# Performance work log

Measured on AMD Instinct MI355X. Metric: run time of the kernel, lower is better.

The kernel has to match this reference:

```python
import jax, jax.numpy as jnp
import numpy as np

N, NFEAT, NHID, NCLASS = 8192, 512, 256, 2
ALPHA = 0.5


def setup_inputs() -> dict:
    key = jax.random.key(0)
    k1, k2, k3, k4, k5 = jax.random.split(key, 5)
    x = jax.random.normal(k1, (N, NFEAT), dtype=jnp.float32)
    adj = jax.random.uniform(k2, (N, N), dtype=jnp.float32)
    # GraphConvolution init: uniform(-stdv, stdv), stdv = 1/sqrt(out_features)
    s1 = 1.0 / np.sqrt(NHID)
    W1 = jax.random.uniform(k3, (NFEAT, NHID), dtype=jnp.float32, minval=-s1, maxval=s1)
    s2 = 1.0 / np.sqrt(NCLASS)
    W2 = jax.random.uniform(k4, (NHID, NCLASS), dtype=jnp.float32, minval=-s2, maxval=s2)
    b2 = jax.random.uniform(k5, (NCLASS,), dtype=jnp.float32, minval=-s2, maxval=s2)
    return {"x": x, "adj": adj, "W1": W1, "W2": W2, "b2": b2}


def _mid_filter_2(adj, alpha):
    # D_row = diag(rowsum^-0.5), D_col = diag(colsum^-0.5); inf -> 0
    d_row = jnp.power(jnp.sum(adj, axis=1), -0.5)
    d_row = jnp.where(jnp.isinf(d_row), 0.0, d_row)
    d_col = jnp.power(jnp.sum(adj, axis=0), -0.5)
    d_col = jnp.where(jnp.isinf(d_col), 0.0, d_col)
    # (adj @ D_col)^T @ D_row)^T == d_row[:,None] * adj * d_col[None,:]
    DAD = d_row[:, None] * adj * d_col[None, :]
    I = jnp.eye(adj.shape[0], dtype=adj.dtype)
    return jnp.matmul(alpha * I - DAD, I + DAD)


def reference(x, adj, W1, W2, b2):
    adj_f = _mid_filter_2(adj, ALPHA)
    # hidden layer (no bias): relu(adj_f @ (x @ W1)); dropout = identity (eval)
    h = jax.nn.relu(jnp.matmul(adj_f, jnp.matmul(x, W1)))
    # output layer (with bias)
    out = jnp.matmul(adj_f, jnp.matmul(h, W2)) + b2
    return jax.nn.log_softmax(out, axis=-1)
```

## Files before the change

kernel.cpp:

```cpp
#include <hip/hip_runtime.h>
#include <hip/hip_bf16.h>

typedef unsigned short u16;
typedef unsigned int u32;
typedef __attribute__((ext_vector_type(8))) short short8;
typedef __attribute__((ext_vector_type(4))) float f32x4;

#define NN 8192
#define NF 512
#define NH 256
#define SPLITZ 8
#define RB 256

__device__ __forceinline__ float bf2f(u32 u) {
  union { u32 i; float f; } v; v.i = u << 16; return v.f;
}
__device__ __forceinline__ u16 f2bf(float f) {
  union { __hip_bfloat16 b; u16 u; } v; v.b = __float2bfloat16(f); return v.u;
}
__device__ __forceinline__ u32 pack2(float a, float b) {
  return (u32)f2bf(a) | ((u32)f2bf(b) << 16);
}

__global__ __launch_bounds__(256) void conv_adj_k(const float* __restrict__ adj,
                                                  u16* __restrict__ adjb,
                                                  float* __restrict__ rowsum_part,
                                                  float* __restrict__ colsum_part) {
  __shared__ float red[4][32];
  const int t = threadIdx.x;
  const int w = t >> 6, lane = t & 63;
  const int s = blockIdx.x;
  const int c0 = s * 2048 + t * 8;
  const int r0 = blockIdx.y * 32;
  float cp[8] = {0.f, 0.f, 0.f, 0.f, 0.f, 0.f, 0.f, 0.f};
  for (int r = 0; r < 32; ++r) {
    const size_t base = (size_t)(r0 + r) * NN + c0;
    float4 v0 = *(const float4*)(adj + base);
    float4 v1 = *(const float4*)(adj + base + 4);
    uint4 pk;
    pk.x = pack2(v0.x, v0.y); pk.y = pack2(v0.z, v0.w);
    pk.z = pack2(v1.x, v1.y); pk.w = pack2(v1.z, v1.w);
    *(uint4*)(adjb + base) = pk;
    cp[0] += v0.x; cp[1] += v0.y; cp[2] += v0.z; cp[3] += v0.w;
    cp[4] += v1.x; cp[5] += v1.y; cp[6] += v1.z; cp[7] += v1.w;
    float rs = (v0.x + v0.y) + (v0.z + v0.w) + ((v1.x + v1.y) + (v1.z + v1.w));
#pragma unroll
    for (int off = 32; off > 0; off >>= 1) rs += __shfl_down(rs, off, 64);
    if (lane == 0) red[w][r] = rs;
  }
  __syncthreads();
  if (t < 32)
    rowsum_part[(size_t)s * NN + r0 + t] =
        (red[0][t] + red[1][t]) + (red[2][t] + red[3][t]);
  float* cdst = colsum_part + (size_t)blockIdx.y * NN + c0;
  *(float4*)cdst = make_float4(cp[0], cp[1], cp[2], cp[3]);
  *(float4*)(cdst + 4) = make_float4(cp[4], cp[5], cp[6], cp[7]);
}

__global__ __launch_bounds__(256) void reduce_sums_k(const float* __restrict__ rowp,
                                                     const float* __restrict__ colp,
                                                     float* __restrict__ drow,
                                                     float* __restrict__ dcol) {
  const int i = blockIdx.x * 256 + threadIdx.x;
  const float rs = (rowp[i] + rowp[NN + i]) + (rowp[2 * NN + i] + rowp[3 * NN + i]);
  drow[i] = (rs > 0.f) ? rsqrtf(rs) : 0.f;
  float cs = 0.f;
#pragma unroll 8
  for (int rb = 0; rb < RB; ++rb) cs += colp[(size_t)rb * NN + i];
  dcol[i] = (cs > 0.f) ? rsqrtf(cs) : 0.f;
}

__global__ __launch_bounds__(256) void convx_k(const float* __restrict__ x,
                                               u16* __restrict__ xb) {
  const size_t i = ((size_t)blockIdx.x * 256 + threadIdx.x) * 8;
  float4 v0 = *(const float4*)(x + i);
  float4 v1 = *(const float4*)(x + i + 4);
  uint4 pk;
  pk.x = pack2(v0.x, v0.y); pk.y = pack2(v0.z, v0.w);
  pk.z = pack2(v1.x, v1.y); pk.w = pack2(v1.z, v1.w);
  *(uint4*)(xb + i) = pk;
}

__global__ __launch_bounds__(256) void convw1_k(const float* __restrict__ in,
                                                u16* __restrict__ out) {
  __shared__ float tile[32][33];
  const int tx = threadIdx.x & 31, ty = threadIdx.x >> 5;
  const int c0 = blockIdx.x * 32;
  const int r0 = blockIdx.y * 32;
#pragma unroll
  for (int d = 0; d < 32; d += 8)
    tile[ty + d][tx] = in[(size_t)(r0 + ty + d) * NH + c0 + tx];
  __syncthreads();
#pragma unroll
  for (int d = 0; d < 32; d += 8)
    out[(size_t)(c0 + ty + d) * NF + r0 + tx] = f2bf(tile[tx][ty + d]);
}

__device__ __forceinline__ void stage128(const u16* __restrict__ A, int lda,
                                         const u16* __restrict__ Bt, int ldb,
                                         int m0, int n0, int kk,
                                         u16* as_, u16* bs_, int tid) {
#pragma unroll
  for (int h = 0; h < 2; ++h) {
    const int slot = tid + h * 256;
    const int row = slot >> 2, kc = slot & 3;
    const u16* srcA = A + (size_t)(m0 + row) * lda + kk + kc * 8;
    __builtin_amdgcn_global_load_lds((const __attribute__((address_space(1))) void*)srcA,
                                     (__attribute__((address_space(3))) void*)(as_ + slot * 8),
                                     16, 0, 0);
    const u16* srcB = Bt + (size_t)(n0 + row) * ldb + kk + kc * 8;
    __builtin_amdgcn_global_load_lds((const __attribute__((address_space(1))) void*)srcB,
                                     (__attribute__((address_space(3))) void*)(bs_ + slot * 8),
                                     16, 0, 0);
  }
}

__global__ __launch_bounds__(256) void gemm_k(const u16* __restrict__ A, int lda,
                                              const u16* __restrict__ Bt, int ldb,
                                              int kChunk, float* __restrict__ out) {
  __shared__ __align__(16) u16 As[2][128 * 32];
  __shared__ __align__(16) u16 Bs[2][128 * 32];
  const int tid = threadIdx.x;
  const int w = tid >> 6, lane = tid & 63;
  const int lq = lane >> 4, lr = lane & 15;
  const int wr = (w >> 1) * 64, wc = (w & 1) * 64;
  const int n0 = blockIdx.x * 128;
  const int m0 = blockIdx.y * 128;
  const int kk0 = blockIdx.z * kChunk;
  const int nk = kChunk >> 5;

  f32x4 acc[4][4] = {};

  stage128(A, lda, Bt, ldb, m0, n0, kk0, As[0], Bs[0], tid);
  for (int kt = 0; kt < nk; ++kt) {
    const int cur = kt & 1;
    __syncthreads();
    if (kt + 1 < nk)
      stage128(A, lda, Bt, ldb, m0, n0, kk0 + ((kt + 1) << 5), As[cur ^ 1], Bs[cur ^ 1], tid);
    short8 a[4], b[4];
#pragma unroll
    for (int i = 0; i < 4; ++i)
      a[i] = *(const short8*)(As[cur] + (wr + i * 16 + lr) * 32 + lq * 8);
#pragma unroll
    for (int i = 0; i < 4; ++i)
      b[i] = *(const short8*)(Bs[cur] + (wc + i * 16 + lr) * 32 + lq * 8);
#pragma unroll
    for (int i = 0; i < 4; ++i)
#pragma unroll
      for (int j = 0; j < 4; ++j)
        acc[i][j] = __builtin_amdgcn_mfma_f32_16x16x32_bf16(a[i], b[j], acc[i][j], 0, 0, 0);
  }

  float* o = out + (size_t)blockIdx.z * ((size_t)NN * NH);
#pragma unroll
  for (int i = 0; i < 4; ++i)
#pragma unroll
    for (int j = 0; j < 4; ++j) {
      const int gn = n0 + wc + j * 16 + lr;
      const int gm0 = m0 + wr + i * 16 + lq * 4;
#pragma unroll
      for (int r = 0; r < 4; ++r)
        o[(size_t)(gm0 + r) * NH + gn] = acc[i][j][r];
    }
}

__device__ __forceinline__ void stage256(const u16* __restrict__ A, int lda,
                                         const u16* __restrict__ Bt, int ldb,
                                         int m0, int kk,
                                         u16* as_, u16* bs_, int tid) {
#pragma unroll
  for (int h = 0; h < 4; ++h) {
    const int slot = tid + h * 512;
    const int row = slot >> 3, kc = (slot & 7) * 8;
    const u16* srcA = A + (size_t)(m0 + row) * lda + kk + kc;
    __builtin_amdgcn_global_load_lds((const __attribute__((address_space(1))) void*)srcA,
                                     (__attribute__((address_space(3))) void*)(as_ + slot * 8),
                                     16, 0, 0);
    const u16* srcB = Bt + (size_t)row * ldb + kk + kc;
    __builtin_amdgcn_global_load_lds((const __attribute__((address_space(1))) void*)srcB,
                                     (__attribute__((address_space(3))) void*)(bs_ + slot * 8),
                                     16, 0, 0);
  }
}

__global__ __launch_bounds__(512, 2) void gemm256_k(const u16* __restrict__ A, int lda,
                                                    const u16* __restrict__ Bt, int ldb,
                                                    int kChunk, float* __restrict__ out) {
  __shared__ __align__(16) u16 As[2][256 * 64];
  __shared__ __align__(16) u16 Bs[2][256 * 64];
  const int tid = threadIdx.x;
  const int w = tid >> 6, lane = tid & 63;
  const int lq = lane >> 4, lr = lane & 15;
  const int wr = (w >> 2) * 128;
  const int wc = (w & 3) * 64;
  const int m0 = blockIdx.x * 256;
  const int kk0 = blockIdx.y * kChunk;
  const int nk = kChunk >> 6;

  f32x4 acc[8][4] = {};

  stage256(A, lda, Bt, ldb, m0, kk0, As[0], Bs[0], tid);
  for (int kt = 0; kt < nk; ++kt) {
    const int cur = kt & 1;
    __syncthreads();
    if (kt + 1 < nk)
      stage256(A, lda, Bt, ldb, m0, kk0 + ((kt + 1) << 6), As[cur ^ 1], Bs[cur ^ 1], tid);
#pragma unroll
    for (int kk2 = 0; kk2 < 2; ++kk2) {
      short8 a[8], b[4];
#pragma unroll
      for (int i = 0; i < 8; ++i)
        a[i] = *(const short8*)(As[cur] + (wr + i * 16 + lr) * 64 + kk2 * 32 + lq * 8);
#pragma unroll
      for (int j = 0; j < 4; ++j)
        b[j] = *(const short8*)(Bs[cur] + (wc + j * 16 + lr) * 64 + kk2 * 32 + lq * 8);
#pragma unroll
      for (int i = 0; i < 8; ++i)
#pragma unroll
        for (int j = 0; j < 4; ++j)
          acc[i][j] = __builtin_amdgcn_mfma_f32_16x16x32_bf16(a[i], b[j], acc[i][j], 0, 0, 0);
    }
  }

  float* o = out + (size_t)blockIdx.y * ((size_t)NN * NH);
#pragma unroll
  for (int i = 0; i < 8; ++i)
#pragma unroll
    for (int j = 0; j < 4; ++j) {
      const int gn = wc + j * 16 + lr;
      const int gm0 = m0 + wr + i * 16 + lq * 4;
#pragma unroll
      for (int r = 0; r < 4; ++r)
        o[(size_t)(gm0 + r) * NH + gn] = acc[i][j][r];
    }
}

__global__ __launch_bounds__(256) void t1_k(const float* __restrict__ P,
                                            const float* __restrict__ dcol,
                                            u16* __restrict__ B1t) {
  __shared__ float tile[32][33];
  const int tx = threadIdx.x & 31, ty = threadIdx.x >> 5;
  const int c0 = blockIdx.x * 32;
  const int r0 = blockIdx.y * 32;
#pragma unroll
  for (int d = 0; d < 32; d += 8) {
    const int rr = r0 + ty + d;
    tile[ty + d][tx] = dcol[rr] * P[(size_t)rr * NH + c0 + tx];
  }
  __syncthreads();
#pragma unroll
  for (int d = 0; d < 32; d += 8)
    B1t[(size_t)(c0 + ty + d) * NN + r0 + tx] = f2bf(tile[tx][ty + d]);
}

__global__ __launch_bounds__(256) void r2_k(const float* __restrict__ Qp,
                                            const float* __restrict__ drow,
                                            const float* __restrict__ dcol,
                                            float* __restrict__ Q1,
                                            u16* __restrict__ B2t) {
  __shared__ float tile[32][33];
  const int tx = threadIdx.x & 31, ty = threadIdx.x >> 5;
  const int c0 = blockIdx.x * 32;
  const int r0 = blockIdx.y * 32;
  const size_t sl = (size_t)NN * NH;
#pragma unroll
  for (int d = 0; d < 32; d += 8) {
    const int rr = r0 + ty + d;
    const size_t idx = (size_t)rr * NH + c0 + tx;
    float s = 0.f;
#pragma unroll
    for (int z = 0; z < SPLITZ; ++z) s += Qp[idx + (size_t)z * sl];
    const float q = drow[rr] * s;
    Q1[idx] = q;
    tile[ty + d][tx] = dcol[rr] * q;
  }
  __syncthreads();
#pragma unroll
  for (int d = 0; d < 32; d += 8)
    B2t[(size_t)(c0 + ty + d) * NN + r0 + tx] = f2bf(tile[tx][ty + d]);
}

__global__ __launch_bounds__(256) void r3_k(const float* __restrict__ Hp,
                                            const float* __restrict__ P,
                                            const float* __restrict__ Q1,
                                            const float* __restrict__ drow,
                                            u16* __restrict__ Hb) {
  const size_t i = ((size_t)blockIdx.x * 256 + threadIdx.x) * 4;
  const int row = (int)(i >> 8);
  const size_t sl = (size_t)NN * NH;
  float4 s = make_float4(0.f, 0.f, 0.f, 0.f);
#pragma unroll
  for (int z = 0; z < SPLITZ; ++z) {
    float4 v = *(const float4*)(Hp + i + (size_t)z * sl);
    s.x += v.x; s.y += v.y; s.z += v.z; s.w += v.w;
  }
  float4 p = *(const float4*)(P + i);
  float4 q = *(const float4*)(Q1 + i);
  const float dr = drow[row];
  const float h0 = fmaxf(0.5f * p.x - 0.5f * q.x - dr * s.x, 0.f);
  const float h1 = fmaxf(0.5f * p.y - 0.5f * q.y - dr * s.y, 0.f);
  const float h2 = fmaxf(0.5f * p.z - 0.5f * q.z - dr * s.z, 0.f);
  const float h3 = fmaxf(0.5f * p.w - 0.5f * q.w - dr * s.w, 0.f);
  uint2 pk;
  pk.x = pack2(h0, h1);
  pk.y = pack2(h2, h3);
  *(uint2*)(Hb + i) = pk;
}

__global__ __launch_bounds__(256) void r_k(const u16* __restrict__ H,
                                           const float* __restrict__ W2,
                                           const float* __restrict__ dcol,
                                           float* __restrict__ R, float* __restrict__ B3) {
  const int w = threadIdx.x >> 6, lane = threadIdx.x & 63;
  const int i = blockIdx.x * 4 + w;
  uint2 hv = *(const uint2*)(H + (size_t)i * NH + lane * 4);
  float4 w01 = *(const float4*)(W2 + lane * 8);
  float4 w23 = *(const float4*)(W2 + lane * 8 + 4);
  const float h0 = bf2f(hv.x & 0xffffu), h1 = bf2f(hv.x >> 16);
  const float h2 = bf2f(hv.y & 0xffffu), h3 = bf2f(hv.y >> 16);
  float a0 = h0 * w01.x + h1 * w01.z + h2 * w23.x + h3 * w23.z;
  float a1 = h0 * w01.y + h1 * w01.w + h2 * w23.y + h3 * w23.w;
#pragma unroll
  for (int off = 32; off > 0; off >>= 1) {
    a0 += __shfl_down(a0, off, 64);
    a1 += __shfl_down(a1, off, 64);
  }
  if (lane == 0) {
    R[i * 2] = a0;
    R[i * 2 + 1] = a1;
    const float dc = dcol[i];
    B3[i * 2] = dc * a0;
    B3[i * 2 + 1] = dc * a1;
  }
}

__global__ __launch_bounds__(256) void gemv_k(
    const u16* __restrict__ adjb, const float* __restrict__ B,
    const float* __restrict__ drow, const float* __restrict__ dcol,
    const float* __restrict__ Rin, const float* __restrict__ S1in,
    const float* __restrict__ b2, float* __restrict__ S1out,
    float* __restrict__ B4, float* __restrict__ outp, int mode) {
  const int i = blockIdx.x;
  const int t = threadIdx.x;
  float a0 = 0.f, a1 = 0.f;
#pragma unroll
  for (int c = 0; c < 4; ++c) {
    const int col = c * 2048 + t * 8;
    uint4 av = *(const uint4*)(adjb + (size_t)i * NN + col);
    const u32* aw = (const u32*)&av;
    float bv[16];
    *(float4*)(bv) = *(const float4*)(B + col * 2);
    *(float4*)(bv + 4) = *(const float4*)(B + col * 2 + 4);
    *(float4*)(bv + 8) = *(const float4*)(B + col * 2 + 8);
    *(float4*)(bv + 12) = *(const float4*)(B + col * 2 + 12);
#pragma unroll
    for (int j = 0; j < 8; ++j) {
      const u32 a = aw[j >> 1];
      const float aval = bf2f((j & 1) ? (a >> 16) : (a & 0xffffu));
      a0 += aval * bv[2 * j];
      a1 += aval * bv[2 * j + 1];
    }
  }
#pragma unroll
  for (int off = 32; off > 0; off >>= 1) {
    a0 += __shfl_down(a0, off, 64);
    a1 += __shfl_down(a1, off, 64);
  }
  __shared__ float red[8];
  const int w = t >> 6, lane = t & 63;
  if (lane == 0) { red[w] = a0; red[4 + w] = a1; }
  __syncthreads();
  if (t == 0) {
    float s0 = (red[0] + red[1]) + (red[2] + red[3]);
    float s1 = (red[4] + red[5]) + (red[6] + red[7]);
    const float dr = drow[i];
    s0 *= dr; s1 *= dr;
    if (mode == 0) {
      S1out[i * 2] = s0;
      S1out[i * 2 + 1] = s1;
      const float dc = dcol[i];
      B4[i * 2] = dc * s0;
      B4[i * 2 + 1] = dc * s1;
    } else {
      const float l0 = 0.5f * Rin[i * 2] - 0.5f * S1in[i * 2] - s0 + b2[0];
      const float l1 = 0.5f * Rin[i * 2 + 1] - 0.5f * S1in[i * 2 + 1] - s1 + b2[1];
      const float m = fmaxf(l0, l1);
      const float lse = m + logf(__expf(l0 - m) + __expf(l1 - m));
      outp[i * 2] = l0 - lse;
      outp[i * 2 + 1] = l1 - lse;
    }
  }
}

extern "C" void kernel_launch(void* const* d_in, const int* in_sizes, int n_in,
                              void* d_out, int out_size, void* d_ws, size_t ws_size,
                              hipStream_t stream) {
  (void)in_sizes; (void)n_in; (void)out_size; (void)ws_size;
  const float* x   = (const float*)d_in[0];
  const float* adj = (const float*)d_in[1];
  const float* W1  = (const float*)d_in[2];
  const float* W2  = (const float*)d_in[3];
  const float* b2  = (const float*)d_in[4];
  float* outp = (float*)d_out;

  char* ws = (char*)d_ws;
  size_t off = 0;
  auto alloc = [&](size_t bytes) -> char* {
    char* p = ws + off;
    off += (bytes + 255) & ~(size_t)255;
    return p;
  };
  u16* adjb  = (u16*)alloc((size_t)NN * NN * 2);
  u16* xb    = (u16*)alloc((size_t)NN * NF * 2);
  u16* W1t   = (u16*)alloc((size_t)NH * NF * 2);
  float* rowp = (float*)alloc((size_t)4 * NN * 4);
  float* colp = (float*)alloc((size_t)RB * NN * 4);
  float* drow = (float*)alloc((size_t)NN * 4);
  float* dcol = (float*)alloc((size_t)NN * 4);
  float* P   = (float*)alloc((size_t)NN * NH * 4);
  u16* B1t   = (u16*)alloc((size_t)NH * NN * 2);
  float* Qp  = (float*)alloc((size_t)SPLITZ * NN * NH * 4);
  float* Q1  = (float*)alloc((size_t)NN * NH * 4);
  u16* B2t   = (u16*)alloc((size_t)NH * NN * 2);
  u16* Hb    = (u16*)alloc((size_t)NN * NH * 2);
  float* R   = (float*)alloc((size_t)NN * 2 * 4);
  float* B3  = (float*)alloc((size_t)NN * 2 * 4);
  float* S1  = (float*)alloc((size_t)NN * 2 * 4);
  float* B4  = (float*)alloc((size_t)NN * 2 * 4);
  float* Hp  = Qp;

  conv_adj_k<<<dim3(4, RB), 256, 0, stream>>>(adj, adjb, rowp, colp);
  reduce_sums_k<<<NN / 256, 256, 0, stream>>>(rowp, colp, drow, dcol);
  convx_k<<<2048, 256, 0, stream>>>(x, xb);
  convw1_k<<<dim3(8, 16), 256, 0, stream>>>(W1, W1t);

  gemm_k<<<dim3(2, 64, 1), 256, 0, stream>>>(xb, NF, W1t, NF, NF, P);
  t1_k<<<dim3(8, 256), 256, 0, stream>>>(P, dcol, B1t);

  gemm256_k<<<dim3(32, SPLITZ), 512, 0, stream>>>(adjb, NN, B1t, NN, NN / SPLITZ, Qp);
  r2_k<<<dim3(8, 256), 256, 0, stream>>>(Qp, drow, dcol, Q1, B2t);

  gemm256_k<<<dim3(32, SPLITZ), 512, 0, stream>>>(adjb, NN, B2t, NN, NN / SPLITZ, Hp);
  r3_k<<<2048, 256, 0, stream>>>(Hp, P, Q1, drow, Hb);

  r_k<<<NN / 4, 256, 0, stream>>>(Hb, W2, dcol, R, B3);
  gemv_k<<<NN, 256, 0, stream>>>(adjb, B3, drow, dcol, nullptr, nullptr, nullptr, S1, B4, nullptr, 0);
  gemv_k<<<NN, 256, 0, stream>>>(adjb, B4, drow, dcol, R, S1, b2, nullptr, nullptr, outp, 1);
}
```

Before: 652.8 us.

## Fuse conversion kernels, merge adj pass with x@W1 GEMM, deepen GEMM pipeline

Merges the x and W1 conversions into one launch, and runs the adj bf16 conversion with row/col sums in the same grid as the x@W1 GEMM so the two independent jobs overlap. The big adj GEMM moves to a 4-stage LDS ring with BK=32, XOR-swizzled LDS layout, explicit vmcnt waits with raw barriers, and setprio around the MFMAs. The H reduction is fused with the W2 projection, so the bf16 H round trip is gone. The hand-written waitcnt counts depend on the exact number of outstanding loads, and the smaller K step adds more barriers per tile.

```diff
diff --git a/kernel.cpp b/kernel.cpp
--- a/kernel.cpp
+++ b/kernel.cpp
@@ -11,6 +11,7 @@
 #define NH 256
 #define SPLITZ 8
 #define RB 256
+#define BKR 32
 
 __device__ __forceinline__ float bf2f(u32 u) {
   union { u32 i; float f; } v; v.i = u << 16; return v.f;
@@ -20,41 +21,6 @@
 }
 __device__ __forceinline__ u32 pack2(float a, float b) {
   return (u32)f2bf(a) | ((u32)f2bf(b) << 16);
-}
-
-__global__ __launch_bounds__(256) void conv_adj_k(const float* __restrict__ adj,
-                                                  u16* __restrict__ adjb,
-                                                  float* __restrict__ rowsum_part,
-                                                  float* __restrict__ colsum_part) {
-  __shared__ float red[4][32];
-  const int t = threadIdx.x;
-  const int w = t >> 6, lane = t & 63;
-  const int s = blockIdx.x;
-  const int c0 = s * 2048 + t * 8;
-  const int r0 = blockIdx.y * 32;
-  float cp[8] = {0.f, 0.f, 0.f, 0.f, 0.f, 0.f, 0.f, 0.f};
-  for (int r = 0; r < 32; ++r) {
-    const size_t base = (size_t)(r0 + r) * NN + c0;
-    float4 v0 = *(const float4*)(adj + base);
-    float4 v1 = *(const float4*)(adj + base + 4);
-    uint4 pk;
-    pk.x = pack2(v0.x, v0.y); pk.y = pack2(v0.z, v0.w);
-    pk.z = pack2(v1.x, v1.y); pk.w = pack2(v1.z, v1.w);
-    *(uint4*)(adjb + base) = pk;
-    cp[0] += v0.x; cp[1] += v0.y; cp[2] += v0.z; cp[3] += v0.w;
-    cp[4] += v1.x; cp[5] += v1.y; cp[6] += v1.z; cp[7] += v1.w;
-    float rs = (v0.x + v0.y) + (v0.z + v0.w) + ((v1.x + v1.y) + (v1.z + v1.w));
-#pragma unroll
-    for (int off = 32; off > 0; off >>= 1) rs += __shfl_down(rs, off, 64);
-    if (lane == 0) red[w][r] = rs;
-  }
-  __syncthreads();
-  if (t < 32)
-    rowsum_part[(size_t)s * NN + r0 + t] =
-        (red[0][t] + red[1][t]) + (red[2][t] + red[3][t]);
-  float* cdst = colsum_part + (size_t)blockIdx.y * NN + c0;
-  *(float4*)cdst = make_float4(cp[0], cp[1], cp[2], cp[3]);
-  *(float4*)(cdst + 4) = make_float4(cp[4], cp[5], cp[6], cp[7]);
 }
 
 __global__ __launch_bounds__(256) void reduce_sums_k(const float* __restrict__ rowp,
@@ -70,30 +36,32 @@
   dcol[i] = (cs > 0.f) ? rsqrtf(cs) : 0.f;
 }
 
-__global__ __launch_bounds__(256) void convx_k(const float* __restrict__ x,
-                                               u16* __restrict__ xb) {
-  const size_t i = ((size_t)blockIdx.x * 256 + threadIdx.x) * 8;
-  float4 v0 = *(const float4*)(x + i);
-  float4 v1 = *(const float4*)(x + i + 4);
-  uint4 pk;
-  pk.x = pack2(v0.x, v0.y); pk.y = pack2(v0.z, v0.w);
-  pk.z = pack2(v1.x, v1.y); pk.w = pack2(v1.z, v1.w);
-  *(uint4*)(xb + i) = pk;
-}
-
-__global__ __launch_bounds__(256) void convw1_k(const float* __restrict__ in,
-                                                u16* __restrict__ out) {
+__global__ __launch_bounds__(256) void convxw1_k(const float* __restrict__ x,
+                                                 u16* __restrict__ xb,
+                                                 const float* __restrict__ W1,
+                                                 u16* __restrict__ W1t) {
   __shared__ float tile[32][33];
-  const int tx = threadIdx.x & 31, ty = threadIdx.x >> 5;
-  const int c0 = blockIdx.x * 32;
-  const int r0 = blockIdx.y * 32;
-#pragma unroll
-  for (int d = 0; d < 32; d += 8)
-    tile[ty + d][tx] = in[(size_t)(r0 + ty + d) * NH + c0 + tx];
-  __syncthreads();
-#pragma unroll
-  for (int d = 0; d < 32; d += 8)
-    out[(size_t)(c0 + ty + d) * NF + r0 + tx] = f2bf(tile[tx][ty + d]);
+  if (blockIdx.x < 2048) {
+    const size_t i = ((size_t)blockIdx.x * 256 + threadIdx.x) * 8;
+    float4 v0 = *(const float4*)(x + i);
+    float4 v1 = *(const float4*)(x + i + 4);
+    uint4 pk;
+    pk.x = pack2(v0.x, v0.y); pk.y = pack2(v0.z, v0.w);
+    pk.z = pack2(v1.x, v1.y); pk.w = pack2(v1.z, v1.w);
+    *(uint4*)(xb + i) = pk;
+  } else {
+    const int blk = blockIdx.x - 2048;
+    const int tx = threadIdx.x & 31, ty = threadIdx.x >> 5;
+    const int c0 = (blk & 7) * 32;
+    const int r0 = (blk >> 3) * 32;
+#pragma unroll
+    for (int d = 0; d < 32; d += 8)
+      tile[ty + d][tx] = W1[(size_t)(r0 + ty + d) * NH + c0 + tx];
+    __syncthreads();
+#pragma unroll
+    for (int d = 0; d < 32; d += 8)
+      W1t[(size_t)(c0 + ty + d) * NF + r0 + tx] = f2bf(tile[tx][ty + d]);
+  }
 }
 
 __device__ __forceinline__ void stage128(const u16* __restrict__ A, int lda,
@@ -115,79 +83,115 @@
   }
 }
 
-__global__ __launch_bounds__(256) void gemm_k(const u16* __restrict__ A, int lda,
-                                              const u16* __restrict__ Bt, int ldb,
-                                              int kChunk, float* __restrict__ out) {
+__global__ __launch_bounds__(256) void mega_k(const float* __restrict__ adj,
+                                              u16* __restrict__ adjb,
+                                              float* __restrict__ rowsum_part,
+                                              float* __restrict__ colsum_part,
+                                              const u16* __restrict__ xb,
+                                              const u16* __restrict__ W1t,
+                                              float* __restrict__ P) {
+  __shared__ float red[4][32];
   __shared__ __align__(16) u16 As[2][128 * 32];
   __shared__ __align__(16) u16 Bs[2][128 * 32];
   const int tid = threadIdx.x;
-  const int w = tid >> 6, lane = tid & 63;
-  const int lq = lane >> 4, lr = lane & 15;
-  const int wr = (w >> 1) * 64, wc = (w & 1) * 64;
-  const int n0 = blockIdx.x * 128;
-  const int m0 = blockIdx.y * 128;
-  const int kk0 = blockIdx.z * kChunk;
-  const int nk = kChunk >> 5;
-
-  f32x4 acc[4][4] = {};
-
-  stage128(A, lda, Bt, ldb, m0, n0, kk0, As[0], Bs[0], tid);
-  for (int kt = 0; kt < nk; ++kt) {
-    const int cur = kt & 1;
+  if (blockIdx.x < 1024) {
+    const int t = tid;
+    const int w = t >> 6, lane = t & 63;
+    const int s = blockIdx.x & 3;
+    const int c0 = s * 2048 + t * 8;
+    const int r0 = (blockIdx.x >> 2) * 32;
+    float cp[8] = {0.f, 0.f, 0.f, 0.f, 0.f, 0.f, 0.f, 0.f};
+    for (int r = 0; r < 32; ++r) {
+      const size_t base = (size_t)(r0 + r) * NN + c0;
+      float4 v0 = *(const float4*)(adj + base);
+      float4 v1 = *(const float4*)(adj + base + 4);
+      uint4 pk;
+      pk.x = pack2(v0.x, v0.y); pk.y = pack2(v0.z, v0.w);
+      pk.z = pack2(v1.x, v1.y); pk.w = pack2(v1.z, v1.w);
+      *(uint4*)(adjb + base) = pk;
+      cp[0] += v0.x; cp[1] += v0.y; cp[2] += v0.z; cp[3] += v0.w;
+      cp[4] += v1.x; cp[5] += v1.y; cp[6] += v1.z; cp[7] += v1.w;
+      float rs = (v0.x + v0.y) + (v0.z + v0.w) + ((v1.x + v1.y) + (v1.z + v1.w));
+#pragma unroll
+      for (int off = 32; off > 0; off >>= 1) rs += __shfl_down(rs, off, 64);
+      if (lane == 0) red[w][r] = rs;
+    }
     __syncthreads();
-    if (kt + 1 < nk)
-      stage128(A, lda, Bt, ldb, m0, n0, kk0 + ((kt + 1) << 5), As[cur ^ 1], Bs[cur ^ 1], tid);
-    short8 a[4], b[4];
+    if (t < 32)
+      rowsum_part[(size_t)s * NN + r0 + t] =
+          (red[0][t] + red[1][t]) + (red[2][t] + red[3][t]);
+    float* cdst = colsum_part + (size_t)(blockIdx.x >> 2) * NN + c0;
+    *(float4*)cdst = make_float4(cp[0], cp[1], cp[2], cp[3]);
+    *(float4*)(cdst + 4) = make_float4(cp[4], cp[5], cp[6], cp[7]);
+  } else {
+    const int blk = blockIdx.x - 1024;
+    const int w = tid >> 6, lane = tid & 63;
+    const int lq = lane >> 4, lr = lane & 15;
+    const int wr = (w >> 1) * 64, wc = (w & 1) * 64;
+    const int n0 = (blk & 1) * 128;
+    const int m0 = (blk >> 1) * 128;
+    const int nk = NF >> 5;
+
+    f32x4 acc[4][4] = {};
+
+    stage128(xb, NF, W1t, NF, m0, n0, 0, As[0], Bs[0], tid);
+    for (int kt = 0; kt < nk; ++kt) {
+      const int cur = kt & 1;
+      __syncthreads();
+      if (kt + 1 < nk)
+        stage128(xb, NF, W1t, NF, m0, n0, (kt + 1) << 5, As[cur ^ 1], Bs[cur ^ 1], tid);
+      short8 a[4], b[4];
+#pragma unroll
+      for (int i = 0; i < 4; ++i)
+        a[i] = *(const short8*)(As[cur] + (wr + i * 16 + lr) * 32 + lq * 8);
+#pragma unroll
+      for (int i = 0; i < 4; ++i)
+        b[i] = *(const short8*)(Bs[cur] + (wc + i * 16 + lr) * 32 + lq * 8);
+#pragma unroll
+      for (int i = 0; i < 4; ++i)
+#pragma unroll
+        for (int j = 0; j < 4; ++j)
+          acc[i][j] = __builtin_amdgcn_mfma_f32_16x16x32_bf16(a[i], b[j], acc[i][j], 0, 0, 0);
+    }
 #pragma unroll
     for (int i = 0; i < 4; ++i)
-      a[i] = *(const short8*)(As[cur] + (wr + i * 16 + lr) * 32 + lq * 8);
-#pragma unroll
-    for (int i = 0; i < 4; ++i)
-      b[i] = *(const short8*)(Bs[cur] + (wc + i * 16 + lr) * 32 + lq * 8);
-#pragma unroll
-    for (int i = 0; i < 4; ++i)
-#pragma unroll
-      for (int j = 0; j < 4; ++j)
-        acc[i][j] = __builtin_amdgcn_mfma_f32_16x16x32_bf16(a[i], b[j], acc[i][j], 0, 0, 0);
-  }
-
-  float* o = out + (size_t)blockIdx.z * ((size_t)NN * NH);
-#pragma unroll
-  for (int i = 0; i < 4; ++i)
-#pragma unroll
-    for (int j = 0; j < 4; ++j) {
-      const int gn = n0 + wc + j * 16 + lr;
-      const int gm0 = m0 + wr + i * 16 + lq * 4;
-#pragma unroll
-      for (int r = 0; r < 4; ++r)
-        o[(size_t)(gm0 + r) * NH + gn] = acc[i][j][r];
-    }
-}
-
-__device__ __forceinline__ void stage256(const u16* __restrict__ A, int lda,
-                                         const u16* __restrict__ Bt, int ldb,
-                                         int m0, int kk,
-                                         u16* as_, u16* bs_, int tid) {
-#pragma unroll
-  for (int h = 0; h < 4; ++h) {
+#pragma unroll
+      for (int j = 0; j < 4; ++j) {
+        const int gn = n0 + wc + j * 16 + lr;
+        const int gm0 = m0 + wr + i * 16 + lq * 4;
+#pragma unroll
+        for (int r = 0; r < 4; ++r)
+          P[(size_t)(gm0 + r) * NH + gn] = acc[i][j][r];
+      }
+  }
+}
+
+__device__ __forceinline__ void stage_r(const u16* __restrict__ A,
+                                        const u16* __restrict__ Bt,
+                                        int m0, int kk,
+                                        u16* as_, u16* bs_, int tid) {
+#pragma unroll
+  for (int h = 0; h < 2; ++h) {
     const int slot = tid + h * 512;
-    const int row = slot >> 3, kc = (slot & 7) * 8;
-    const u16* srcA = A + (size_t)(m0 + row) * lda + kk + kc;
+    const int row = slot >> 2, c16 = slot & 3;
+    const int sc16 = c16 ^ (row & 3);
+    const u16* srcA = A + (size_t)(m0 + row) * NN + kk + sc16 * 8;
     __builtin_amdgcn_global_load_lds((const __attribute__((address_space(1))) void*)srcA,
                                      (__attribute__((address_space(3))) void*)(as_ + slot * 8),
                                      16, 0, 0);
-    const u16* srcB = Bt + (size_t)row * ldb + kk + kc;
+    const u16* srcB = Bt + (size_t)row * NN + kk + sc16 * 8;
     __builtin_amdgcn_global_load_lds((const __attribute__((address_space(1))) void*)srcB,
                                      (__attribute__((address_space(3))) void*)(bs_ + slot * 8),
                                      16, 0, 0);
   }
 }
 
-__global__ __launch_bounds__(512, 2) void gemm256_k(const u16* __restrict__ A, int lda,
-                                                    const u16* __restrict__ Bt, int ldb,
-                                                    int kChunk, float* __restrict__ out) {
-  __shared__ __align__(16) u16 As[2][256 * 64];
-  __shared__ __align__(16) u16 Bs[2][256 * 64];
+__global__ __launch_bounds__(512, 2) void gemm256r_k(const u16* __restrict__ A,
+                                                     const u16* __restrict__ Bt,
+                                                     int kChunk,
+                                                     float* __restrict__ out) {
+  __shared__ __align__(16) u16 As[4][256 * BKR];
+  __shared__ __align__(16) u16 Bs[4][256 * BKR];
   const int tid = threadIdx.x;
   const int w = tid >> 6, lane = tid & 63;
   const int lq = lane >> 4, lr = lane & 15;
@@ -195,31 +199,42 @@
   const int wc = (w & 3) * 64;
   const int m0 = blockIdx.x * 256;
   const int kk0 = blockIdx.y * kChunk;
-  const int nk = kChunk >> 6;
+  const int nk = kChunk / BKR;
 
   f32x4 acc[8][4] = {};
 
-  stage256(A, lda, Bt, ldb, m0, kk0, As[0], Bs[0], tid);
+  stage_r(A, Bt, m0, kk0, As[0], Bs[0], tid);
+  stage_r(A, Bt, m0, kk0 + BKR, As[1], Bs[1], tid);
+  stage_r(A, Bt, m0, kk0 + 2 * BKR, As[2], Bs[2], tid);
+
   for (int kt = 0; kt < nk; ++kt) {
-    const int cur = kt & 1;
-    __syncthreads();
-    if (kt + 1 < nk)
-      stage256(A, lda, Bt, ldb, m0, kk0 + ((kt + 1) << 6), As[cur ^ 1], Bs[cur ^ 1], tid);
-#pragma unroll
-    for (int kk2 = 0; kk2 < 2; ++kk2) {
-      short8 a[8], b[4];
-#pragma unroll
-      for (int i = 0; i < 8; ++i)
-        a[i] = *(const short8*)(As[cur] + (wr + i * 16 + lr) * 64 + kk2 * 32 + lq * 8);
+    if (kt + 2 < nk)      asm volatile("s_waitcnt vmcnt(8)" ::: "memory");
+    else if (kt + 1 < nk) asm volatile("s_waitcnt vmcnt(4)" ::: "memory");
+    else                  asm volatile("s_waitcnt vmcnt(0)" ::: "memory");
+    __builtin_amdgcn_s_barrier();
+    __builtin_amdgcn_sched_barrier(0);
+    if (kt + 3 < nk)
+      stage_r(A, Bt, m0, kk0 + (kt + 3) * BKR, As[(kt + 3) & 3], Bs[(kt + 3) & 3], tid);
+    const u16* as_ = As[kt & 3];
+    const u16* bs_ = Bs[kt & 3];
+    short8 a[8], b[4];
+#pragma unroll
+    for (int i = 0; i < 8; ++i) {
+      const int ar = wr + i * 16 + lr;
+      a[i] = *(const short8*)(as_ + ar * BKR + ((lq ^ (ar & 3)) << 3));
+    }
+#pragma unroll
+    for (int j = 0; j < 4; ++j) {
+      const int br = wc + j * 16 + lr;
+      b[j] = *(const short8*)(bs_ + br * BKR + ((lq ^ (br & 3)) << 3));
+    }
+    __builtin_amdgcn_s_setprio(1);
+#pragma unroll
+    for (int i = 0; i < 8; ++i)
 #pragma unroll
       for (int j = 0; j < 4; ++j)
-        b[j] = *(const short8*)(Bs[cur] + (wc + j * 16 + lr) * 64 + kk2 * 32 + lq * 8);
-#pragma unroll
-      for (int i = 0; i < 8; ++i)
-#pragma unroll
-        for (int j = 0; j < 4; ++j)
-          acc[i][j] = __builtin_amdgcn_mfma_f32_16x16x32_bf16(a[i], b[j], acc[i][j], 0, 0, 0);
-    }
+        acc[i][j] = __builtin_amdgcn_mfma_f32_16x16x32_bf16(a[i], b[j], acc[i][j], 0, 0, 0);
+    __builtin_amdgcn_s_setprio(0);
   }
 
   float* o = out + (size_t)blockIdx.y * ((size_t)NN * NH);
@@ -235,9 +250,9 @@
     }
 }
 
-__global__ __launch_bounds__(256) void t1_k(const float* __restrict__ P,
+__global__ __launch_bounds__(256) void t1_k(const float* __restrict__ S,
                                             const float* __restrict__ dcol,
-                                            u16* __restrict__ B1t) {
+                                            u16* __restrict__ Bt) {
   __shared__ float tile[32][33];
   const int tx = threadIdx.x & 31, ty = threadIdx.x >> 5;
   const int c0 = blockIdx.x * 32;
@@ -245,12 +260,12 @@
 #pragma unroll
   for (int d = 0; d < 32; d += 8) {
     const int rr = r0 + ty + d;
-    tile[ty + d][tx] = dcol[rr] * P[(size_t)rr * NH + c0 + tx];
+    tile[ty + d][tx] = dcol[rr] * S[(size_t)rr * NH + c0 + tx];
   }
   __syncthreads();
 #pragma unroll
   for (int d = 0; d < 32; d += 8)
-    B1t[(size_t)(c0 + ty + d) * NN + r0 + tx] = f2bf(tile[tx][ty + d]);
+    Bt[(size_t)(c0 + ty + d) * NN + r0 + tx] = f2bf(tile[tx][ty + d]);
 }
 
 __global__ __launch_bounds__(256) void r2_k(const float* __restrict__ Qp,
@@ -280,44 +295,33 @@
     B2t[(size_t)(c0 + ty + d) * NN + r0 + tx] = f2bf(tile[tx][ty + d]);
 }
 
-__global__ __launch_bounds__(256) void r3_k(const float* __restrict__ Hp,
-                                            const float* __restrict__ P,
-                                            const float* __restrict__ Q1,
-                                            const float* __restrict__ drow,
-                                            u16* __restrict__ Hb) {
-  const size_t i = ((size_t)blockIdx.x * 256 + threadIdx.x) * 4;
-  const int row = (int)(i >> 8);
+__global__ __launch_bounds__(256) void r3r_k(const float* __restrict__ Hp,
+                                             const float* __restrict__ P,
+                                             const float* __restrict__ Q1,
+                                             const float* __restrict__ drow,
+                                             const float* __restrict__ W2,
+                                             const float* __restrict__ dcol,
+                                             float* __restrict__ R,
+                                             float* __restrict__ B3) {
+  const int w = threadIdx.x >> 6, lane = threadIdx.x & 63;
+  const int i = blockIdx.x * 4 + w;
+  const size_t base = (size_t)i * NH + lane * 4;
   const size_t sl = (size_t)NN * NH;
   float4 s = make_float4(0.f, 0.f, 0.f, 0.f);
 #pragma unroll
   for (int z = 0; z < SPLITZ; ++z) {
-    float4 v = *(const float4*)(Hp + i + (size_t)z * sl);
+    float4 v = *(const float4*)(Hp + base + (size_t)z * sl);
     s.x += v.x; s.y += v.y; s.z += v.z; s.w += v.w;
   }
-  float4 p = *(const float4*)(P + i);
-  float4 q = *(const float4*)(Q1 + i);
-  const float dr = drow[row];
+  float4 p = *(const float4*)(P + base);
+  float4 q = *(const float4*)(Q1 + base);
+  const float dr = drow[i];
   const float h0 = fmaxf(0.5f * p.x - 0.5f * q.x - dr * s.x, 0.f);
   const float h1 = fmaxf(0.5f * p.y - 0.5f * q.y - dr * s.y, 0.f);
   const float h2 = fmaxf(0.5f * p.z - 0.5f * q.z - dr * s.z, 0.f);
   const float h3 = fmaxf(0.5f * p.w - 0.5f * q.w - dr * s.w, 0.f);
-  uint2 pk;
-  pk.x = pack2(h0, h1);
-  pk.y = pack2(h2, h3);
-  *(uint2*)(Hb + i) = pk;
-}
-
-__global__ __launch_bounds__(256) void r_k(const u16* __restrict__ H,
-                                           const float* __restrict__ W2,
-                                           const float* __restrict__ dcol,
-                                           float* __restrict__ R, float* __restrict__ B3) {
-  const int w = threadIdx.x >> 6, lane = threadIdx.x & 63;
-  const int i = blockIdx.x * 4 + w;
-  uint2 hv = *(const uint2*)(H + (size_t)i * NH + lane * 4);
   float4 w01 = *(const float4*)(W2 + lane * 8);
   float4 w23 = *(const float4*)(W2 + lane * 8 + 4);
-  const float h0 = bf2f(hv.x & 0xffffu), h1 = bf2f(hv.x >> 16);
-  const float h2 = bf2f(hv.y & 0xffffu), h3 = bf2f(hv.y >> 16);
   float a0 = h0 * w01.x + h1 * w01.z + h2 * w23.x + h3 * w23.z;
   float a1 = h0 * w01.y + h1 * w01.w + h2 * w23.y + h3 * w23.w;
 #pragma unroll
@@ -422,28 +426,24 @@
   float* Qp  = (float*)alloc((size_t)SPLITZ * NN * NH * 4);
   float* Q1  = (float*)alloc((size_t)NN * NH * 4);
   u16* B2t   = (u16*)alloc((size_t)NH * NN * 2);
-  u16* Hb    = (u16*)alloc((size_t)NN * NH * 2);
   float* R   = (float*)alloc((size_t)NN * 2 * 4);
   float* B3  = (float*)alloc((size_t)NN * 2 * 4);
   float* S1  = (float*)alloc((size_t)NN * 2 * 4);
   float* B4  = (float*)alloc((size_t)NN * 2 * 4);
   float* Hp  = Qp;
 
-  conv_adj_k<<<dim3(4, RB), 256, 0, stream>>>(adj, adjb, rowp, colp);
+  convxw1_k<<<2176, 256, 0, stream>>>(x, xb, W1, W1t);
+  mega_k<<<1152, 256, 0, stream>>>(adj, adjb, rowp, colp, xb, W1t, P);
   reduce_sums_k<<<NN / 256, 256, 0, stream>>>(rowp, colp, drow, dcol);
-  convx_k<<<2048, 256, 0, stream>>>(x, xb);
-  convw1_k<<<dim3(8, 16), 256, 0, stream>>>(W1, W1t);
-
-  gemm_k<<<dim3(2, 64, 1), 256, 0, stream>>>(xb, NF, W1t, NF, NF, P);
   t1_k<<<dim3(8, 256), 256, 0, stream>>>(P, dcol, B1t);
 
-  gemm256_k<<<dim3(32, SPLITZ), 512, 0, stream>>>(adjb, NN, B1t, NN, NN / SPLITZ, Qp);
+  gemm256r_k<<<dim3(32, SPLITZ), 512, 0, stream>>>(adjb, B1t, NN / SPLITZ, Qp);
   r2_k<<<dim3(8, 256), 256, 0, stream>>>(Qp, drow, dcol, Q1, B2t);
 
-  gemm256_k<<<dim3(32, SPLITZ), 512, 0, stream>>>(adjb, NN, B2t, NN, NN / SPLITZ, Hp);
-  r3_k<<<2048, 256, 0, stream>>>(Hp, P, Q1, drow, Hb);
-
-  r_k<<<NN / 4, 256, 0, stream>>>(Hb, W2, dcol, R, B3);
+  gemm256r_k<<<dim3(32, SPLITZ), 512, 0, stream>>>(adjb, B2t, NN / SPLITZ, Hp);
+
+  r3r_k<<<NN / 4, 256, 0, stream>>>(Hp, P, Q1, drow, W2, dcol, R, B3);
+
   gemv_k<<<NN, 256, 0, stream>>>(adjb, B3, drow, dcol, nullptr, nullptr, nullptr, S1, B4, nullptr, 0);
   gemv_k<<<NN, 256, 0, stream>>>(adjb, B4, drow, dcol, R, S1, b2, nullptr, nullptr, outp, 1);
 }
```

Result: no change. 648.4 us (median of 2 runs) (-0.7%).
